# Kernel optimization log

Measured on AMD Instinct MI355X. Metric: run time of the kernel, lower is better.

Reference implementation:

```python
import jax, jax.numpy as jnp
import numpy as np

EPS = 1e-6

def setup_inputs() -> dict:
    key = jax.random.key(0)
    k1, k2 = jax.random.split(key)
    pred_map = jax.random.uniform(k1, (64, 512, 512), dtype=jnp.float32)
    true_map = jax.random.uniform(k2, (64, 512, 512), dtype=jnp.float32)
    return {"pred_map": pred_map, "true_map": true_map}

def reference(pred_map, true_map):
    # per-sample normalize over all non-batch dims, then KL(true || pred), mean over batch
    B = pred_map.shape[0]
    pred = (pred_map + EPS).reshape(B, -1)
    true = (true_map + EPS).reshape(B, -1)
    pred = pred / jnp.sum(pred, axis=1, keepdims=True)
    true = true / jnp.sum(true, axis=1, keepdims=True)
    kl = jnp.sum(true * jnp.log(true / pred), axis=1)  # [B]
    return jnp.mean(kl)
```

## Files before the change

kernel.cpp:

```cpp
#include <hip/hip_runtime.h>
#include <hip/hip_bf16.h>

#define EPS 1e-6f

constexpr int B = 64;
constexpr int NPB = 512 * 512;
constexpr int CHUNK = 4096;
constexpr int BLOCKS_PER_BATCH = NPB / CHUNK;
constexpr int NBLK = B * BLOCKS_PER_BATCH;
constexpr int THREADS = 256;
constexpr int OPS_PER_WAVE = CHUNK / 256 / 4;

__device__ __forceinline__ float waveReduce(float v) {
    #pragma unroll
    for (int off = 32; off > 0; off >>= 1) v += __shfl_down(v, off, 64);
    return v;
}

__device__ __forceinline__ void stage16(const float* g, float* l) {
    __builtin_amdgcn_global_load_lds(
        (const __attribute__((address_space(1))) void*)g,
        (__attribute__((address_space(3))) void*)l, 16, 0, 0);
}

__global__ __launch_bounds__(THREADS) void kl_partial(
        const float* __restrict__ pred, const float* __restrict__ truem,
        float* __restrict__ ws) {
    __shared__ float lds_p[CHUNK];
    __shared__ float lds_t[CHUNK];

    const size_t base = (size_t)blockIdx.x * CHUNK;
    const int wave = threadIdx.x >> 6;
    const int lane = threadIdx.x & 63;

    #pragma unroll
    for (int j = 0; j < OPS_PER_WAVE; ++j) {
        const int blkoff = (wave * OPS_PER_WAVE + j) * 256;
        stage16(pred + base + blkoff + lane * 4, lds_p + blkoff);
    }
    #pragma unroll
    for (int j = 0; j < OPS_PER_WAVE; ++j) {
        const int blkoff = (wave * OPS_PER_WAVE + j) * 256;
        stage16(truem + base + blkoff + lane * 4, lds_t + blkoff);
    }
    __syncthreads();

    const float4* lp = (const float4*)lds_p;
    const float4* lt = (const float4*)lds_t;

    float sp = 0.f, st = 0.f, s = 0.f;
    #pragma unroll
    for (int j = 0; j < CHUNK / 4 / THREADS; ++j) {
        float4 p = lp[threadIdx.x + j * THREADS];
        float4 t = lt[threadIdx.x + j * THREADS];
        sp += (p.x + p.y) + (p.z + p.w);
        st += (t.x + t.y) + (t.z + t.w);
        float px = p.x + EPS, py = p.y + EPS, pz = p.z + EPS, pw = p.w + EPS;
        float tx = t.x + EPS, ty = t.y + EPS, tz = t.z + EPS, tw = t.w + EPS;
        s += tx * (__logf(tx) - __logf(px));
        s += ty * (__logf(ty) - __logf(py));
        s += tz * (__logf(tz) - __logf(pz));
        s += tw * (__logf(tw) - __logf(pw));
    }

    sp = waveReduce(sp);
    st = waveReduce(st);
    s  = waveReduce(s);

    __shared__ float red[3][THREADS / 64];
    if (lane == 0) { red[0][wave] = sp; red[1][wave] = st; red[2][wave] = s; }
    __syncthreads();
    if (threadIdx.x == 0) {
        float a0 = 0.f, a1 = 0.f, a2 = 0.f;
        #pragma unroll
        for (int w = 0; w < THREADS / 64; ++w) {
            a0 += red[0][w]; a1 += red[1][w]; a2 += red[2][w];
        }
        ws[blockIdx.x]            = a0;
        ws[NBLK + blockIdx.x]     = a1;
        ws[2 * NBLK + blockIdx.x] = a2;
    }
}

__global__ __launch_bounds__(64) void kl_final(
        const float* __restrict__ ws, float* __restrict__ out) {
    const int b = threadIdx.x;
    float Sp = 0.f, St = 0.f, S = 0.f;
    #pragma unroll 8
    for (int k = 0; k < BLOCKS_PER_BATCH; ++k) {
        const int idx = b * BLOCKS_PER_BATCH + k;
        Sp += ws[idx];
        St += ws[NBLK + idx];
        S  += ws[2 * NBLK + idx];
    }
    const float epsN = (float)NPB * EPS;
    Sp += epsN;
    St += epsN;
    float kl = S / St + logf(Sp / St);
    kl = waveReduce(kl);
    if (b == 0) out[0] = kl * (1.0f / B);
}

extern "C" void kernel_launch(void* const* d_in, const int* in_sizes, int n_in,
                              void* d_out, int out_size, void* d_ws, size_t ws_size,
                              hipStream_t stream) {
    const float* pred  = (const float*)d_in[0];
    const float* truem = (const float*)d_in[1];
    float* out = (float*)d_out;
    float* ws  = (float*)d_ws;

    kl_partial<<<NBLK, THREADS, 0, stream>>>(pred, truem, ws);
    kl_final<<<1, 64, 0, stream>>>(ws, out);
}
```

Before: 143.0 us.

## Double-buffer per-wave LDS staging with persistent loop over chunks

Replaces the one-chunk-per-block design (4096 blocks) with 1024 blocks in which each wave streams its own contiguous slice through a two-slot LDS buffer. Loads for the next chunk are issued before computing the current one, with explicit vmcnt waits to overlap memory with the log math, and block-level syncs are removed. Per-wave partials are written directly, and the final kernel uses 256 threads to reduce the now 4x larger workspace. This adds a dependence on hand-written vmcnt counts and lowers the number of waves in flight.

```diff
diff --git a/kernel.cpp b/kernel.cpp
--- a/kernel.cpp
+++ b/kernel.cpp
@@ -5,11 +5,15 @@
 
 constexpr int B = 64;
 constexpr int NPB = 512 * 512;
-constexpr int CHUNK = 4096;
-constexpr int BLOCKS_PER_BATCH = NPB / CHUNK;
+constexpr int THREADS = 256;
+constexpr int WPB = THREADS / 64;
+constexpr int BLOCKS_PER_BATCH = 16;
 constexpr int NBLK = B * BLOCKS_PER_BATCH;
-constexpr int THREADS = 256;
-constexpr int OPS_PER_WAVE = CHUNK / 256 / 4;
+constexpr int ELEM_PER_BLOCK = NPB / BLOCKS_PER_BATCH;
+constexpr int ELEM_PER_WAVE = ELEM_PER_BLOCK / WPB;
+constexpr int CHUNK = 512;
+constexpr int NCHUNK = ELEM_PER_WAVE / CHUNK;
+constexpr int NW = NBLK * WPB;
 
 __device__ __forceinline__ float waveReduce(float v) {
     #pragma unroll
@@ -26,79 +30,95 @@
 __global__ __launch_bounds__(THREADS) void kl_partial(
         const float* __restrict__ pred, const float* __restrict__ truem,
         float* __restrict__ ws) {
-    __shared__ float lds_p[CHUNK];
-    __shared__ float lds_t[CHUNK];
+    __shared__ float lds[WPB][2][2 * CHUNK];
 
-    const size_t base = (size_t)blockIdx.x * CHUNK;
     const int wave = threadIdx.x >> 6;
     const int lane = threadIdx.x & 63;
-
-    #pragma unroll
-    for (int j = 0; j < OPS_PER_WAVE; ++j) {
-        const int blkoff = (wave * OPS_PER_WAVE + j) * 256;
-        stage16(pred + base + blkoff + lane * 4, lds_p + blkoff);
-    }
-    #pragma unroll
-    for (int j = 0; j < OPS_PER_WAVE; ++j) {
-        const int blkoff = (wave * OPS_PER_WAVE + j) * 256;
-        stage16(truem + base + blkoff + lane * 4, lds_t + blkoff);
-    }
-    __syncthreads();
-
-    const float4* lp = (const float4*)lds_p;
-    const float4* lt = (const float4*)lds_t;
+    const size_t wbase = (size_t)blockIdx.x * ELEM_PER_BLOCK
+                       + (size_t)wave * ELEM_PER_WAVE;
+    const float* gp = pred + wbase;
+    const float* gt = truem + wbase;
 
     float sp = 0.f, st = 0.f, s = 0.f;
+
+    auto issue = [&](int c) {
+        const float* p = gp + c * CHUNK;
+        const float* t = gt + c * CHUNK;
+        float* lp = &lds[wave][c & 1][0];
+        float* lt = &lds[wave][c & 1][CHUNK];
+        stage16(p + lane * 4,       lp);
+        stage16(p + 256 + lane * 4, lp + 256);
+        stage16(t + lane * 4,       lt);
+        stage16(t + 256 + lane * 4, lt + 256);
+    };
+
+    auto compute = [&](int c) {
+        const float4* p4 = (const float4*)&lds[wave][c & 1][0];
+        const float4* t4 = (const float4*)&lds[wave][c & 1][CHUNK];
+        #pragma unroll
+        for (int j = 0; j < 2; ++j) {
+            float4 p = p4[lane + j * 64];
+            float4 t = t4[lane + j * 64];
+            sp += (p.x + p.y) + (p.z + p.w);
+            st += (t.x + t.y) + (t.z + t.w);
+            float px = p.x + EPS, py = p.y + EPS, pz = p.z + EPS, pw = p.w + EPS;
+            float tx = t.x + EPS, ty = t.y + EPS, tz = t.z + EPS, tw = t.w + EPS;
+            s += tx * (__logf(tx) - __logf(px));
+            s += ty * (__logf(ty) - __logf(py));
+            s += tz * (__logf(tz) - __logf(pz));
+            s += tw * (__logf(tw) - __logf(pw));
+        }
+    };
+
+    issue(0);
     #pragma unroll
-    for (int j = 0; j < CHUNK / 4 / THREADS; ++j) {
-        float4 p = lp[threadIdx.x + j * THREADS];
-        float4 t = lt[threadIdx.x + j * THREADS];
-        sp += (p.x + p.y) + (p.z + p.w);
-        st += (t.x + t.y) + (t.z + t.w);
-        float px = p.x + EPS, py = p.y + EPS, pz = p.z + EPS, pw = p.w + EPS;
-        float tx = t.x + EPS, ty = t.y + EPS, tz = t.z + EPS, tw = t.w + EPS;
-        s += tx * (__logf(tx) - __logf(px));
-        s += ty * (__logf(ty) - __logf(py));
-        s += tz * (__logf(tz) - __logf(pz));
-        s += tw * (__logf(tw) - __logf(pw));
+    for (int c = 1; c < NCHUNK; ++c) {
+        issue(c);
+        asm volatile("s_waitcnt vmcnt(4)" ::: "memory");
+        compute(c - 1);
     }
+    asm volatile("s_waitcnt vmcnt(0)" ::: "memory");
+    compute(NCHUNK - 1);
 
     sp = waveReduce(sp);
     st = waveReduce(st);
     s  = waveReduce(s);
-
-    __shared__ float red[3][THREADS / 64];
-    if (lane == 0) { red[0][wave] = sp; red[1][wave] = st; red[2][wave] = s; }
-    __syncthreads();
-    if (threadIdx.x == 0) {
-        float a0 = 0.f, a1 = 0.f, a2 = 0.f;
-        #pragma unroll
-        for (int w = 0; w < THREADS / 64; ++w) {
-            a0 += red[0][w]; a1 += red[1][w]; a2 += red[2][w];
-        }
-        ws[blockIdx.x]            = a0;
-        ws[NBLK + blockIdx.x]     = a1;
-        ws[2 * NBLK + blockIdx.x] = a2;
+    if (lane == 0) {
+        const int idx = blockIdx.x * WPB + wave;
+        ws[idx]          = sp;
+        ws[NW + idx]     = st;
+        ws[2 * NW + idx] = s;
     }
 }
 
-__global__ __launch_bounds__(64) void kl_final(
+__global__ __launch_bounds__(256) void kl_final(
         const float* __restrict__ ws, float* __restrict__ out) {
-    const int b = threadIdx.x;
+    const int b = threadIdx.x & 63;
+    const int q = threadIdx.x >> 6;
     float Sp = 0.f, St = 0.f, S = 0.f;
-    #pragma unroll 8
-    for (int k = 0; k < BLOCKS_PER_BATCH; ++k) {
-        const int idx = b * BLOCKS_PER_BATCH + k;
+    #pragma unroll
+    for (int k = 0; k < 16; ++k) {
+        const int idx = b * 64 + q * 16 + k;
         Sp += ws[idx];
-        St += ws[NBLK + idx];
-        S  += ws[2 * NBLK + idx];
+        St += ws[NW + idx];
+        S  += ws[2 * NW + idx];
     }
-    const float epsN = (float)NPB * EPS;
-    Sp += epsN;
-    St += epsN;
-    float kl = S / St + logf(Sp / St);
-    kl = waveReduce(kl);
-    if (b == 0) out[0] = kl * (1.0f / B);
+    __shared__ float r[3][4][64];
+    r[0][q][b] = Sp; r[1][q][b] = St; r[2][q][b] = S;
+    __syncthreads();
+    if (threadIdx.x < 64) {
+        const int bb = threadIdx.x;
+        float sp = 0.f, stt = 0.f, ss = 0.f;
+        #pragma unroll
+        for (int qq = 0; qq < 4; ++qq) {
+            sp += r[0][qq][bb]; stt += r[1][qq][bb]; ss += r[2][qq][bb];
+        }
+        const float epsN = (float)NPB * EPS;
+        sp += epsN; stt += epsN;
+        float kl = ss / stt + logf(sp / stt);
+        kl = waveReduce(kl);
+        if (bb == 0) out[0] = kl * (1.0f / B);
+    }
 }
 
 extern "C" void kernel_launch(void* const* d_in, const int* in_sizes, int n_in,
@@ -110,5 +130,5 @@
     float* ws  = (float*)d_ws;
 
     kl_partial<<<NBLK, THREADS, 0, stream>>>(pred, truem, ws);
-    kl_final<<<1, 64, 0, stream>>>(ws, out);
+    kl_final<<<1, 256, 0, stream>>>(ws, out);
 }
```

After: 149.3 us. 1.04x slower.
